# Kernel tuning notes

Measured on AMD Instinct MI355X. Metric: run time of the kernel, lower is better.

The kernel has to match this reference:

```python
import jax, jax.numpy as jnp
import numpy as np

B, N, D, E, H = 8, 256, 128, 32, 4
HD = D // H
EPS = 1e-5


def setup_inputs() -> dict:
    key = jax.random.key(0)
    ks = jax.random.split(key, 20)
    idx = jnp.arange(N)

    h = jax.random.normal(ks[0], (B, N, D), dtype=jnp.float32)
    adj = (jax.random.uniform(ks[1], (B, N, N)) < 0.5).astype(jnp.float32)
    adj = adj.at[:, idx, idx].set(1.0)
    edge_features = jax.random.normal(ks[2], (B, N, N, E), dtype=jnp.float32)
    src_mask = (jax.random.uniform(ks[3], (B, N, N)) < 0.7).astype(jnp.float32)
    src_mask = src_mask.at[:, idx, idx].set(1.0)

    s = 1.0 / np.sqrt(D)
    se = 1.0 / np.sqrt(E)
    p = {
        "gcn_w": jax.random.normal(ks[4], (D, D)) * s,
        "gcn_b": jnp.zeros((D,)),
        "edge_w": jax.random.normal(ks[5], (D, E)) * se,
        "edge_b": jnp.zeros((D,)),
        "wq": jax.random.normal(ks[6], (D, D)) * s,
        "wk": jax.random.normal(ks[7], (D, D)) * s,
        "wv": jax.random.normal(ks[8], (D, D)) * s,
        "bq": jnp.zeros((D,)),
        "bk": jnp.zeros((D,)),
        "bv": jnp.zeros((D,)),
        "out_w": jax.random.normal(ks[9], (D, D)) * s,
        "out_b": jnp.zeros((D,)),
        "ln_g": jnp.ones((D,)),
        "ln_b": jnp.zeros((D,)),
    }
    return {"h": h, "adj": adj, "edge_features": edge_features, "src_mask": src_mask, **p}


def reference(h, adj, edge_features, src_mask,
              gcn_w, gcn_b, edge_w, edge_b,
              wq, wk, wv, bq, bk, bv, out_w, out_b, ln_g, ln_b):
    b, n, d = h.shape

    # --- GCN branch: degree-normalized aggregation with self-loops ---
    adj_sl = adj + jnp.eye(n, dtype=h.dtype)[None]          # (B,N,N)
    deg = adj_sl.sum(-1, keepdims=True)                      # (B,N,1)
    h_agg = jnp.einsum('bnm,bmd->bnd', adj_sl, h) / deg
    h_gcn = h_agg @ gcn_w.T + gcn_b                          # (B,N,D)

    # --- edge-conditioned key/value: h_ij = h_j + edge_emb ---
    edge_emb = jnp.einsum('bnme,de->bnmd', edge_features, edge_w) + edge_b
    h_ij = h[:, None, :, :] + edge_emb                       # (B,N,N,D)

    # key padding mask: True where edge absent (masked)
    masked = (adj * src_mask) == 0                           # (B,N,N)

    # --- multi-head attention, one query per node ---
    q = (h @ wq.T + bq).reshape(b, n, H, HD)                 # (B,N,H,HD)
    k = (jnp.einsum('bnmd,ed->bnme', h_ij, wk) + bk).reshape(b, n, n, H, HD)
    v = (jnp.einsum('bnmd,ed->bnme', h_ij, wv) + bv).reshape(b, n, n, H, HD)

    scores = jnp.einsum('bnhd,bnmhd->bnhm', q, k) / np.sqrt(HD)  # (B,N,H,N)
    scores = jnp.where(masked[:, :, None, :], -jnp.inf, scores)
    attn = jax.nn.softmax(scores, axis=-1)
    o = jnp.einsum('bnhm,bnmhd->bnhd', attn, v).reshape(b, n, d)
    o = o @ out_w.T + out_b                                  # (B,N,D)

    # residual + layernorm (dropout is identity in eval)
    x = h + o
    mu = x.mean(-1, keepdims=True)
    var = ((x - mu) ** 2).mean(-1, keepdims=True)
    h_attn = ln_g * (x - mu) / jnp.sqrt(var + EPS) + ln_b

    return h_gcn + h_attn
```

## Files before the change

### kernel.cpp

```cpp
#include <hip/hip_runtime.h>
#include <hip/hip_bf16.h>

#define OFF_WQT 0
#define OFF_WKT 16384
#define OFF_WVT 32768
#define OFF_OWT 49152
#define OFF_GWT 65536
#define OFF_WKE 81920
#define OFF_WVE 86016
#define OFF_KB  90112
#define OFF_VB  90240
#define OFF_SC  90368
#define OFF_QS  98560
#define OFF_QE  360704
#define OFF_HA  622848
#define OFF_O   884992
#define OFF_K0  1147136
#define OFF_V0  1278208

static __device__ __forceinline__ float bflo(unsigned int w){
  union { unsigned int u; float f; } x; x.u = w << 16; return x.f;
}
static __device__ __forceinline__ float bfhi(unsigned int w){
  union { unsigned int u; float f; } x; x.u = w & 0xffff0000u; return x.f;
}
static __device__ __forceinline__ unsigned short f2bf(float f){
  union { float f; unsigned int u; } x; x.f = f;
  unsigned int r = (x.u + 0x7fffu + ((x.u >> 16) & 1u)) >> 16;
  return (unsigned short)r;
}

__global__ __launch_bounds__(256) void prep_kernel(
    const float* __restrict__ wq, const float* __restrict__ wk,
    const float* __restrict__ wv, const float* __restrict__ out_w,
    const float* __restrict__ gcn_w, const float* __restrict__ edge_w,
    const float* __restrict__ edge_b, const float* __restrict__ bk,
    const float* __restrict__ bv, float* __restrict__ ws)
{
  int blk = blockIdx.x, t = threadIdx.x;
  if (blk < 320) {
    int w = blk >> 6;
    int e0 = (blk & 63) * 256 + t;
    const float* src = (w==0) ? wq : (w==1) ? wk : (w==2) ? wv : (w==3) ? out_w : gcn_w;
    float* dst = ws + ((w==0) ? OFF_WQT : (w==1) ? OFF_WKT : (w==2) ? OFF_WVT
                      : (w==3) ? OFF_OWT : OFF_GWT);
    int k = e0 >> 7, d = e0 & 127;
    dst[e0] = src[d*128 + k];
  } else if (blk < 352) {
    int idx = blk - 320;
    int which = idx >> 4;
    int e0 = (idx & 15) * 256 + t;
    int d = e0 >> 5, e = e0 & 31;
    const float* W = which ? wv : wk;
    float acc = 0.f;
    #pragma unroll 4
    for (int k2 = 0; k2 < 128; ++k2) acc += W[d*128+k2] * edge_w[k2*32+e];
    ws[(which ? OFF_WVE : OFF_WKE) + e0] = acc;
  } else {
    int d = t & 127;
    const float* W  = (t < 128) ? wk : wv;
    const float* bb = (t < 128) ? bk : bv;
    float acc = bb[d];
    #pragma unroll 4
    for (int k2 = 0; k2 < 128; ++k2) acc += W[d*128+k2] * edge_b[k2];
    ws[((t < 128) ? OFF_KB : OFF_VB) + d] = acc;
  }
}

__global__ __launch_bounds__(256) void proj_kernel(
    const float* __restrict__ h, const float* __restrict__ bq,
    float* __restrict__ ws)
{
  __shared__ float part1[2][8][128];
  __shared__ float part2[2][8][128];
  __shared__ float part3[2][8][128];
  __shared__ float qrow[8*132];

  int t = threadIdx.x;
  int d = t & 127;
  int kh = __builtin_amdgcn_readfirstlane(t >> 7);
  int r0 = blockIdx.x * 8;

  const float* wqT = ws + OFF_WQT;
  const float* wkT = ws + OFF_WKT;
  const float* wvT = ws + OFF_WVT;

  float aq[8] = {0,0,0,0,0,0,0,0};
  float ak[8] = {0,0,0,0,0,0,0,0};
  float av[8] = {0,0,0,0,0,0,0,0};

  for (int kk = 0; kk < 64; ++kk) {
    int k = kh*64 + kk;
    float qw = wqT[k*128 + d];
    float kw = wkT[k*128 + d];
    float vw = wvT[k*128 + d];
    #pragma unroll
    for (int i = 0; i < 8; ++i) {
      float hv = h[(r0+i)*128 + k];
      aq[i] += qw * hv;
      ak[i] += kw * hv;
      av[i] += vw * hv;
    }
  }
  #pragma unroll
  for (int i = 0; i < 8; ++i) {
    part1[kh][i][d] = aq[i];
    part2[kh][i][d] = ak[i];
    part3[kh][i][d] = av[i];
  }
  __syncthreads();

  unsigned short* K0 = (unsigned short*)(ws + OFF_K0);
  unsigned short* V0 = (unsigned short*)(ws + OFF_V0);
  if (t < 128) {
    const float inv = 0.17677669529663687f;
    #pragma unroll
    for (int i = 0; i < 8; ++i) {
      float q  = (part1[0][i][d] + part1[1][i][d] + bq[d]) * inv;
      float k0 = part2[0][i][d] + part2[1][i][d];
      float v0 = part3[0][i][d] + part3[1][i][d];
      ws[OFF_QS + (r0+i)*128 + d] = q;
      qrow[i*132 + d] = q;
      K0[(r0+i)*128 + d] = f2bf(k0);
      V0[(r0+i)*128 + d] = f2bf(v0);
    }
  }
  __syncthreads();

  const float* Wke = ws + OFF_WKE;
  #pragma unroll
  for (int rep = 0; rep < 4; ++rep) {
    int flat = rep*256 + t;
    int i = flat >> 7, he = flat & 127;
    int hh = he >> 5, e = he & 31;
    float acc = 0.f;
    #pragma unroll
    for (int j = 0; j < 32; ++j)
      acc += Wke[(hh*32+j)*32 + e] * qrow[i*132 + hh*32 + j];
    ws[OFF_QE + (r0+i)*128 + he] = acc;
  }
  if (t < 32) {
    int i = t >> 2, hh = t & 3;
    float acc = 0.f;
    #pragma unroll
    for (int j = 0; j < 32; ++j)
      acc += qrow[i*132 + hh*32 + j] * ws[OFF_KB + hh*32 + j];
    ws[OFF_SC + (r0+i)*4 + hh] = acc;
  }
}

__global__ __launch_bounds__(256) void gcn_kernel(
    const float* __restrict__ h, const float* __restrict__ adj,
    float* __restrict__ ws)
{
  __shared__ float part[2][8][128];
  __shared__ float dpart[2][8];

  int t = threadIdx.x;
  int d = t & 127;
  int mh = __builtin_amdgcn_readfirstlane(t >> 7);
  int b = blockIdx.x >> 5;
  int n0 = (blockIdx.x & 31) * 8;

  float acc[8] = {0,0,0,0,0,0,0,0};
  float deg[8] = {0,0,0,0,0,0,0,0};
  for (int mm = 0; mm < 128; ++mm) {
    int m = mh*128 + mm;
    float hv = h[(b*256 + m)*128 + d];
    #pragma unroll
    for (int i = 0; i < 8; ++i) {
      float a = adj[(b*256 + n0 + i)*256 + m] + ((m == n0 + i) ? 1.0f : 0.0f);
      acc[i] += a * hv;
      deg[i] += a;
    }
  }
  #pragma unroll
  for (int i = 0; i < 8; ++i) part[mh][i][d] = acc[i];
  if (d == 0) {
    #pragma unroll
    for (int i = 0; i < 8; ++i) dpart[mh][i] = deg[i];
  }
  __syncthreads();
  if (t < 128) {
    #pragma unroll
    for (int i = 0; i < 8; ++i) {
      float s  = part[0][i][d] + part[1][i][d];
      float dg = dpart[0][i] + dpart[1][i];
      ws[OFF_HA + (b*256 + n0 + i)*128 + d] = s / dg;
    }
  }
}

__global__ __launch_bounds__(256) void attn_kernel(
    const float* __restrict__ edge, const float* __restrict__ adj,
    const float* __restrict__ srcm, const float* __restrict__ ws,
    float* __restrict__ obuf)
{
  __shared__ float e_lds[256*36];
  __shared__ float s_lds[4*264];
  __shared__ float red[8];
  __shared__ float part[16*132];
  __shared__ float ebar[128];

  int t  = threadIdx.x;
  int bn = blockIdx.x;
  int b  = bn >> 8;

  const float* qs = ws + OFF_QS + (size_t)bn*128;
  const float* qe = ws + OFF_QE + (size_t)bn*128;
  const float* sc = ws + OFF_SC + (size_t)bn*4;
  const unsigned short* K0 = (const unsigned short*)(ws + OFF_K0);
  const unsigned short* V0 = (const unsigned short*)(ws + OFF_V0);

  int m = t;
  float4 ev[8];
  {
    const float4* ep = (const float4*)(edge + ((size_t)bn*256 + (size_t)m)*32);
    #pragma unroll
    for (int j = 0; j < 8; ++j) ev[j] = ep[j];
    float* erow = e_lds + m*36;
    #pragma unroll
    for (int j = 0; j < 8; ++j) ((float4*)erow)[j] = ev[j];
  }

  float s4[4];
  {
    const uint4* kv = (const uint4*)(K0 + (size_t)(b*256 + m)*128);
    #pragma unroll
    for (int hh = 0; hh < 4; ++hh) {
      float acc = sc[hh];
      #pragma unroll
      for (int q4 = 0; q4 < 4; ++q4) {
        uint4 kw = kv[hh*4 + q4];
        const float* qp = qs + hh*32 + q4*8;
        acc += qp[0]*bflo(kw.x) + qp[1]*bfhi(kw.x)
             + qp[2]*bflo(kw.y) + qp[3]*bfhi(kw.y)
             + qp[4]*bflo(kw.z) + qp[5]*bfhi(kw.z)
             + qp[6]*bflo(kw.w) + qp[7]*bfhi(kw.w);
      }
      const float* qep = qe + hh*32;
      #pragma unroll
      for (int j = 0; j < 8; ++j) {
        acc += qep[4*j+0]*ev[j].x + qep[4*j+1]*ev[j].y
             + qep[4*j+2]*ev[j].z + qep[4*j+3]*ev[j].w;
      }
      s4[hh] = acc;
    }
    float ma = adj[(size_t)bn*256 + m];
    float ms = srcm[(size_t)bn*256 + m];
    if (ma * ms == 0.0f) { s4[0] = s4[1] = s4[2] = s4[3] = -1e30f; }
    #pragma unroll
    for (int hh = 0; hh < 4; ++hh) s_lds[hh*264 + m] = s4[hh];
  }
  __syncthreads();

  {
    int wvh = t >> 6, ln = t & 63;
    float v0 = s_lds[wvh*264 + ln];
    float v1 = s_lds[wvh*264 + ln + 64];
    float v2 = s_lds[wvh*264 + ln + 128];
    float v3 = s_lds[wvh*264 + ln + 192];
    float mx = fmaxf(fmaxf(v0, v1), fmaxf(v2, v3));
    #pragma unroll
    for (int off = 32; off > 0; off >>= 1) mx = fmaxf(mx, __shfl_down(mx, off));
    mx = __shfl(mx, 0);
    float sm = __expf(v0-mx) + __expf(v1-mx) + __expf(v2-mx) + __expf(v3-mx);
    #pragma unroll
    for (int off = 32; off > 0; off >>= 1) sm += __shfl_down(sm, off);
    if (ln == 0) { red[wvh] = mx; red[4+wvh] = 1.0f / sm; }
  }
  __syncthreads();

  {
    #pragma unroll
    for (int hh = 0; hh < 4; ++hh) {
      float a = __expf(s4[hh] - red[hh]) * red[4+hh];
      s_lds[hh*264 + m] = a;
    }
  }
  __syncthreads();

  {
    int ms = t >> 5, hh = (t >> 3) & 3, e4 = t & 7;
    float4 acc = {0,0,0,0};
    for (int jm = 0; jm < 32; ++jm) {
      int mm = ms*32 + jm;
      float a = s_lds[hh*264 + mm];
      float4 evv = *(const float4*)(e_lds + mm*36 + e4*4);
      acc.x += a*evv.x; acc.y += a*evv.y; acc.z += a*evv.z; acc.w += a*evv.w;
    }
    *(float4*)(part + ms*132 + hh*32 + e4*4) = acc;
  }
  __syncthreads();
  if (t < 128) {
    float s2 = 0.f;
    #pragma unroll
    for (int ms = 0; ms < 8; ++ms) s2 += part[ms*132 + t];
    ebar[t] = s2;
  }
  __syncthreads();

  {
    int ms = t >> 4, hh = (t >> 2) & 3, dg = t & 3;
    float a0=0,a1=0,a2=0,a3=0,a4=0,a5=0,a6=0,a7=0;
    const uint4* vb = (const uint4*)(V0 + (size_t)b*256*128);
    int colq = hh*4 + dg;
    for (int jm = 0; jm < 16; ++jm) {
      int mm = ms*16 + jm;
      float a = s_lds[hh*264 + mm];
      uint4 vw = vb[mm*16 + colq];
      a0 += a*bflo(vw.x); a1 += a*bfhi(vw.x);
      a2 += a*bflo(vw.y); a3 += a*bfhi(vw.y);
      a4 += a*bflo(vw.z); a5 += a*bfhi(vw.z);
      a6 += a*bflo(vw.w); a7 += a*bfhi(vw.w);
    }
    float* pp = part + ms*132 + hh*32 + dg*8;
    pp[0]=a0; pp[1]=a1; pp[2]=a2; pp[3]=a3; pp[4]=a4; pp[5]=a5; pp[6]=a6; pp[7]=a7;
  }
  __syncthreads();

  if (t < 128) {
    float s2 = 0.f;
    #pragma unroll
    for (int ms = 0; ms < 16; ++ms) s2 += part[ms*132 + t];
    int hh = t >> 5;
    float acc = s2 + ws[OFF_VB + t];
    const float* wve = ws + OFF_WVE + t*32;
    #pragma unroll
    for (int e = 0; e < 32; ++e) acc += wve[e] * ebar[hh*32 + e];
    obuf[(size_t)bn*128 + t] = acc;
  }
}

__global__ __launch_bounds__(256) void final_kernel(
    const float* __restrict__ h, const float* __restrict__ ws,
    const float* __restrict__ out_b, const float* __restrict__ ln_g,
    const float* __restrict__ ln_b, const float* __restrict__ gcn_b,
    float* __restrict__ out)
{
  __shared__ float p1[2][8][128];
  __shared__ float p2[2][8][128];
  __shared__ float xl[8*132];
  __shared__ float stat[16];

  int t = threadIdx.x;
  int d = t & 127;
  int kh = __builtin_amdgcn_readfirstlane(t >> 7);
  int r0 = blockIdx.x * 8;

  const float* owT = ws + OFF_OWT;
  const float* gwT = ws + OFF_GWT;
  const float* ob  = ws + OFF_O;
  const float* ha  = ws + OFF_HA;

  float xa[8] = {0,0,0,0,0,0,0,0};
  float ga[8] = {0,0,0,0,0,0,0,0};
  for (int kk = 0; kk < 64; ++kk) {
    int k = kh*64 + kk;
    float ow = owT[k*128 + d];
    float gw = gwT[k*128 + d];
    #pragma unroll
    for (int i = 0; i < 8; ++i) {
      xa[i] += ow * ob[(r0+i)*128 + k];
      ga[i] += gw * ha[(r0+i)*128 + k];
    }
  }
  #pragma unroll
  for (int i = 0; i < 8; ++i) { p1[kh][i][d] = xa[i]; p2[kh][i][d] = ga[i]; }
  __syncthreads();

  float gtot[8];
  if (t < 128) {
    #pragma unroll
    for (int i = 0; i < 8; ++i) {
      float x = p1[0][i][d] + p1[1][i][d] + out_b[d] + h[(r0+i)*128 + d];
      xl[i*132 + d] = x;
      gtot[i] = p2[0][i][d] + p2[1][i][d];
    }
  }
  __syncthreads();

  {
    int i = t >> 5, l = t & 31;
    float s = 0.f, ss = 0.f;
    #pragma unroll
    for (int j = 0; j < 4; ++j) {
      float x = xl[i*132 + l + 32*j];
      s += x; ss += x*x;
    }
    #pragma unroll
    for (int off = 16; off > 0; off >>= 1) {
      s  += __shfl_down(s,  off, 32);
      ss += __shfl_down(ss, off, 32);
    }
    if (l == 0) {
      float mu  = s * (1.0f/128.0f);
      float var = ss * (1.0f/128.0f) - mu*mu;
      stat[i]   = mu;
      stat[8+i] = rsqrtf(var + 1e-5f);
    }
  }
  __syncthreads();

  if (t < 128) {
    #pragma unroll
    for (int i = 0; i < 8; ++i) {
      float mu = stat[i], rs = stat[8+i];
      float x  = xl[i*132 + d];
      out[(r0+i)*128 + d] = ln_g[d]*(x-mu)*rs + ln_b[d] + gtot[i] + gcn_b[d];
    }
  }
}

extern "C" void kernel_launch(void* const* d_in, const int* in_sizes, int n_in,
                              void* d_out, int out_size, void* d_ws, size_t ws_size,
                              hipStream_t stream) {
  (void)in_sizes; (void)n_in; (void)out_size; (void)ws_size;
  const float* h     = (const float*)d_in[0];
  const float* adj   = (const float*)d_in[1];
  const float* edge  = (const float*)d_in[2];
  const float* srcm  = (const float*)d_in[3];
  const float* gcn_w = (const float*)d_in[4];
  const float* gcn_b = (const float*)d_in[5];
  const float* edge_w= (const float*)d_in[6];
  const float* edge_b= (const float*)d_in[7];
  const float* wq    = (const float*)d_in[8];
  const float* wk    = (const float*)d_in[9];
  const float* wv    = (const float*)d_in[10];
  const float* bq    = (const float*)d_in[11];
  const float* bk    = (const float*)d_in[12];
  const float* bv    = (const float*)d_in[13];
  const float* out_w = (const float*)d_in[14];
  const float* out_b = (const float*)d_in[15];
  const float* ln_g  = (const float*)d_in[16];
  const float* ln_b  = (const float*)d_in[17];

  float* ws  = (float*)d_ws;
  float* out = (float*)d_out;

  prep_kernel<<<353, 256, 0, stream>>>(wq, wk, wv, out_w, gcn_w, edge_w, edge_b, bk, bv, ws);
  proj_kernel<<<256, 256, 0, stream>>>(h, bq, ws);
  gcn_kernel<<<256, 256, 0, stream>>>(h, adj, ws);
  attn_kernel<<<2048, 256, 0, stream>>>(edge, adj, srcm, ws, ws + OFF_O);
  final_kernel<<<256, 256, 0, stream>>>(h, ws, out_b, ln_g, ln_b, gcn_b, out);
}
```

Measured before the change: 229.2 us.

## Fuse GCN into final kernel, merge attention reductions, bf16 edge tile in LDS

Removes the separate GCN kernel and computes the degree-normalized aggregation inside the final kernel, so the h_agg workspace round-trip and one launch go away. The attention kernel stores edge features in LDS as bf16 and runs the edge-weighted and V reductions in one loop with fewer barriers, with a launch-bounds occupancy hint. Projection and final kernels switch to 4 rows per block with twice as many blocks, and h and adj rows are staged in LDS. The bf16 edge features add rounding error to the attention output, and the final kernel now carries the full GCN aggregation work.

```diff
diff --git a/kernel.cpp b/kernel.cpp
--- a/kernel.cpp
+++ b/kernel.cpp
@@ -13,7 +13,6 @@
 #define OFF_SC  90368
 #define OFF_QS  98560
 #define OFF_QE  360704
-#define OFF_HA  622848
 #define OFF_O   884992
 #define OFF_K0  1147136
 #define OFF_V0  1278208
@@ -71,23 +70,27 @@
     const float* __restrict__ h, const float* __restrict__ bq,
     float* __restrict__ ws)
 {
-  __shared__ float part1[2][8][128];
-  __shared__ float part2[2][8][128];
-  __shared__ float part3[2][8][128];
-  __shared__ float qrow[8*132];
+  __shared__ float h_lds[512];
+  __shared__ float p1[2][4][128];
+  __shared__ float p2[2][4][128];
+  __shared__ float p3[2][4][128];
+  __shared__ float qrow[4*132];
 
   int t = threadIdx.x;
   int d = t & 127;
-  int kh = __builtin_amdgcn_readfirstlane(t >> 7);
-  int r0 = blockIdx.x * 8;
+  int kh = t >> 7;
+  int r0 = blockIdx.x * 4;
+
+  if (t < 128) ((float4*)h_lds)[t] = ((const float4*)(h + (size_t)r0*128))[t];
+  __syncthreads();
 
   const float* wqT = ws + OFF_WQT;
   const float* wkT = ws + OFF_WKT;
   const float* wvT = ws + OFF_WVT;
 
-  float aq[8] = {0,0,0,0,0,0,0,0};
-  float ak[8] = {0,0,0,0,0,0,0,0};
-  float av[8] = {0,0,0,0,0,0,0,0};
+  float aq[4] = {0,0,0,0};
+  float ak[4] = {0,0,0,0};
+  float av[4] = {0,0,0,0};
 
   for (int kk = 0; kk < 64; ++kk) {
     int k = kh*64 + kk;
@@ -95,18 +98,18 @@
     float kw = wkT[k*128 + d];
     float vw = wvT[k*128 + d];
     #pragma unroll
-    for (int i = 0; i < 8; ++i) {
-      float hv = h[(r0+i)*128 + k];
+    for (int i = 0; i < 4; ++i) {
+      float hv = h_lds[i*128 + k];
       aq[i] += qw * hv;
       ak[i] += kw * hv;
       av[i] += vw * hv;
     }
   }
   #pragma unroll
-  for (int i = 0; i < 8; ++i) {
-    part1[kh][i][d] = aq[i];
-    part2[kh][i][d] = ak[i];
-    part3[kh][i][d] = av[i];
+  for (int i = 0; i < 4; ++i) {
+    p1[kh][i][d] = aq[i];
+    p2[kh][i][d] = ak[i];
+    p3[kh][i][d] = av[i];
   }
   __syncthreads();
 
@@ -115,21 +118,21 @@
   if (t < 128) {
     const float inv = 0.17677669529663687f;
     #pragma unroll
-    for (int i = 0; i < 8; ++i) {
-      float q  = (part1[0][i][d] + part1[1][i][d] + bq[d]) * inv;
-      float k0 = part2[0][i][d] + part2[1][i][d];
-      float v0 = part3[0][i][d] + part3[1][i][d];
-      ws[OFF_QS + (r0+i)*128 + d] = q;
+    for (int i = 0; i < 4; ++i) {
+      float q  = (p1[0][i][d] + p1[1][i][d] + bq[d]) * inv;
+      float k0 = p2[0][i][d] + p2[1][i][d];
+      float v0 = p3[0][i][d] + p3[1][i][d];
+      ws[OFF_QS + (size_t)(r0+i)*128 + d] = q;
       qrow[i*132 + d] = q;
-      K0[(r0+i)*128 + d] = f2bf(k0);
-      V0[(r0+i)*128 + d] = f2bf(v0);
+      K0[(size_t)(r0+i)*128 + d] = f2bf(k0);
+      V0[(size_t)(r0+i)*128 + d] = f2bf(v0);
     }
   }
   __syncthreads();
 
   const float* Wke = ws + OFF_WKE;
   #pragma unroll
-  for (int rep = 0; rep < 4; ++rep) {
+  for (int rep = 0; rep < 2; ++rep) {
     int flat = rep*256 + t;
     int i = flat >> 7, he = flat & 127;
     int hh = he >> 5, e = he & 31;
@@ -137,70 +140,29 @@
     #pragma unroll
     for (int j = 0; j < 32; ++j)
       acc += Wke[(hh*32+j)*32 + e] * qrow[i*132 + hh*32 + j];
-    ws[OFF_QE + (r0+i)*128 + he] = acc;
-  }
-  if (t < 32) {
+    ws[OFF_QE + (size_t)(r0+i)*128 + he] = acc;
+  }
+  if (t < 16) {
     int i = t >> 2, hh = t & 3;
     float acc = 0.f;
     #pragma unroll
     for (int j = 0; j < 32; ++j)
       acc += qrow[i*132 + hh*32 + j] * ws[OFF_KB + hh*32 + j];
-    ws[OFF_SC + (r0+i)*4 + hh] = acc;
-  }
-}
-
-__global__ __launch_bounds__(256) void gcn_kernel(
-    const float* __restrict__ h, const float* __restrict__ adj,
-    float* __restrict__ ws)
-{
-  __shared__ float part[2][8][128];
-  __shared__ float dpart[2][8];
-
-  int t = threadIdx.x;
-  int d = t & 127;
-  int mh = __builtin_amdgcn_readfirstlane(t >> 7);
-  int b = blockIdx.x >> 5;
-  int n0 = (blockIdx.x & 31) * 8;
-
-  float acc[8] = {0,0,0,0,0,0,0,0};
-  float deg[8] = {0,0,0,0,0,0,0,0};
-  for (int mm = 0; mm < 128; ++mm) {
-    int m = mh*128 + mm;
-    float hv = h[(b*256 + m)*128 + d];
-    #pragma unroll
-    for (int i = 0; i < 8; ++i) {
-      float a = adj[(b*256 + n0 + i)*256 + m] + ((m == n0 + i) ? 1.0f : 0.0f);
-      acc[i] += a * hv;
-      deg[i] += a;
-    }
-  }
-  #pragma unroll
-  for (int i = 0; i < 8; ++i) part[mh][i][d] = acc[i];
-  if (d == 0) {
-    #pragma unroll
-    for (int i = 0; i < 8; ++i) dpart[mh][i] = deg[i];
-  }
-  __syncthreads();
-  if (t < 128) {
-    #pragma unroll
-    for (int i = 0; i < 8; ++i) {
-      float s  = part[0][i][d] + part[1][i][d];
-      float dg = dpart[0][i] + dpart[1][i];
-      ws[OFF_HA + (b*256 + n0 + i)*128 + d] = s / dg;
-    }
-  }
-}
-
-__global__ __launch_bounds__(256) void attn_kernel(
+    ws[OFF_SC + (size_t)(r0+i)*4 + hh] = acc;
+  }
+}
+
+__global__ __launch_bounds__(256, 4) void attn_kernel(
     const float* __restrict__ edge, const float* __restrict__ adj,
     const float* __restrict__ srcm, const float* __restrict__ ws,
     float* __restrict__ obuf)
 {
-  __shared__ float e_lds[256*36];
-  __shared__ float s_lds[4*264];
+  __shared__ unsigned int e_bf[256*18];
+  __shared__ float s_lds[1028];
+  __shared__ float part4[8*132];
+  __shared__ float part5[8*132];
+  __shared__ float ebar[128];
   __shared__ float red[8];
-  __shared__ float part[16*132];
-  __shared__ float ebar[128];
 
   int t  = threadIdx.x;
   int bn = blockIdx.x;
@@ -210,17 +172,24 @@
   const float* qe = ws + OFF_QE + (size_t)bn*128;
   const float* sc = ws + OFF_SC + (size_t)bn*4;
   const unsigned short* K0 = (const unsigned short*)(ws + OFF_K0);
-  const unsigned short* V0 = (const unsigned short*)(ws + OFF_V0);
+  const unsigned int*  V0u = (const unsigned int*)(ws + OFF_V0);
 
   int m = t;
+  float ma = adj[(size_t)bn*256 + m];
+  float msk = srcm[(size_t)bn*256 + m];
   float4 ev[8];
   {
     const float4* ep = (const float4*)(edge + ((size_t)bn*256 + (size_t)m)*32);
     #pragma unroll
     for (int j = 0; j < 8; ++j) ev[j] = ep[j];
-    float* erow = e_lds + m*36;
-    #pragma unroll
-    for (int j = 0; j < 8; ++j) ((float4*)erow)[j] = ev[j];
+    unsigned int* erow = e_bf + m*18;
+    #pragma unroll
+    for (int j = 0; j < 8; ++j) {
+      uint2 pk;
+      pk.x = (unsigned int)f2bf(ev[j].x) | ((unsigned int)f2bf(ev[j].y) << 16);
+      pk.y = (unsigned int)f2bf(ev[j].z) | ((unsigned int)f2bf(ev[j].w) << 16);
+      *(uint2*)(erow + j*2) = pk;
+    }
   }
 
   float s4[4];
@@ -246,20 +215,18 @@
       }
       s4[hh] = acc;
     }
-    float ma = adj[(size_t)bn*256 + m];
-    float ms = srcm[(size_t)bn*256 + m];
-    if (ma * ms == 0.0f) { s4[0] = s4[1] = s4[2] = s4[3] = -1e30f; }
-    #pragma unroll
-    for (int hh = 0; hh < 4; ++hh) s_lds[hh*264 + m] = s4[hh];
+    if (ma * msk == 0.0f) { s4[0] = s4[1] = s4[2] = s4[3] = -1e30f; }
+    #pragma unroll
+    for (int hh = 0; hh < 4; ++hh) s_lds[hh*257 + m] = s4[hh];
   }
   __syncthreads();
 
   {
     int wvh = t >> 6, ln = t & 63;
-    float v0 = s_lds[wvh*264 + ln];
-    float v1 = s_lds[wvh*264 + ln + 64];
-    float v2 = s_lds[wvh*264 + ln + 128];
-    float v3 = s_lds[wvh*264 + ln + 192];
+    float v0 = s_lds[wvh*257 + ln];
+    float v1 = s_lds[wvh*257 + ln + 64];
+    float v2 = s_lds[wvh*257 + ln + 128];
+    float v3 = s_lds[wvh*257 + ln + 192];
     float mx = fmaxf(fmaxf(v0, v1), fmaxf(v2, v3));
     #pragma unroll
     for (int off = 32; off > 0; off >>= 1) mx = fmaxf(mx, __shfl_down(mx, off));
@@ -271,58 +238,46 @@
   }
   __syncthreads();
 
-  {
-    #pragma unroll
-    for (int hh = 0; hh < 4; ++hh) {
-      float a = __expf(s4[hh] - red[hh]) * red[4+hh];
-      s_lds[hh*264 + m] = a;
-    }
-  }
-  __syncthreads();
-
-  {
-    int ms = t >> 5, hh = (t >> 3) & 3, e4 = t & 7;
-    float4 acc = {0,0,0,0};
+  #pragma unroll
+  for (int hh = 0; hh < 4; ++hh)
+    s_lds[hh*257 + m] = __expf(s4[hh] - red[hh]) * red[4+hh];
+  __syncthreads();
+
+  {
+    int ms  = t >> 5;
+    int hh4 = (t >> 3) & 3, e4 = t & 7;
+    int c   = t & 31,  hh5 = c >> 3;
+    float p4x=0,p4y=0,p4z=0,p4w=0;
+    float p5x=0,p5y=0,p5z=0,p5w=0;
+    const unsigned int* vrow = V0u + (size_t)b*256*64;
     for (int jm = 0; jm < 32; ++jm) {
       int mm = ms*32 + jm;
-      float a = s_lds[hh*264 + mm];
-      float4 evv = *(const float4*)(e_lds + mm*36 + e4*4);
-      acc.x += a*evv.x; acc.y += a*evv.y; acc.z += a*evv.z; acc.w += a*evv.w;
-    }
-    *(float4*)(part + ms*132 + hh*32 + e4*4) = acc;
-  }
-  __syncthreads();
-  if (t < 128) {
-    float s2 = 0.f;
-    #pragma unroll
-    for (int ms = 0; ms < 8; ++ms) s2 += part[ms*132 + t];
-    ebar[t] = s2;
-  }
-  __syncthreads();
-
-  {
-    int ms = t >> 4, hh = (t >> 2) & 3, dg = t & 3;
-    float a0=0,a1=0,a2=0,a3=0,a4=0,a5=0,a6=0,a7=0;
-    const uint4* vb = (const uint4*)(V0 + (size_t)b*256*128);
-    int colq = hh*4 + dg;
-    for (int jm = 0; jm < 16; ++jm) {
-      int mm = ms*16 + jm;
-      float a = s_lds[hh*264 + mm];
-      uint4 vw = vb[mm*16 + colq];
-      a0 += a*bflo(vw.x); a1 += a*bfhi(vw.x);
-      a2 += a*bflo(vw.y); a3 += a*bfhi(vw.y);
-      a4 += a*bflo(vw.z); a5 += a*bfhi(vw.z);
-      a6 += a*bflo(vw.w); a7 += a*bfhi(vw.w);
-    }
-    float* pp = part + ms*132 + hh*32 + dg*8;
-    pp[0]=a0; pp[1]=a1; pp[2]=a2; pp[3]=a3; pp[4]=a4; pp[5]=a5; pp[6]=a6; pp[7]=a7;
-  }
-  __syncthreads();
-
-  if (t < 128) {
-    float s2 = 0.f;
-    #pragma unroll
-    for (int ms = 0; ms < 16; ++ms) s2 += part[ms*132 + t];
+      float a4 = s_lds[hh4*257 + mm];
+      uint2 w = *(const uint2*)(e_bf + mm*18 + e4*2);
+      p4x += a4*bflo(w.x); p4y += a4*bfhi(w.x);
+      p4z += a4*bflo(w.y); p4w += a4*bfhi(w.y);
+      float a5 = s_lds[hh5*257 + mm];
+      uint2 vv = *(const uint2*)(vrow + (size_t)mm*64 + c*2);
+      p5x += a5*bflo(vv.x); p5y += a5*bfhi(vv.x);
+      p5z += a5*bflo(vv.y); p5w += a5*bfhi(vv.y);
+    }
+    float4 f4; f4.x=p4x; f4.y=p4y; f4.z=p4z; f4.w=p4w;
+    *(float4*)(part4 + ms*132 + hh4*32 + e4*4) = f4;
+    float4 f5; f5.x=p5x; f5.y=p5y; f5.z=p5z; f5.w=p5w;
+    *(float4*)(part5 + ms*132 + c*4) = f5;
+  }
+  __syncthreads();
+
+  float s2 = 0.f;
+  if (t < 128) {
+    float se = 0.f;
+    #pragma unroll
+    for (int g = 0; g < 8; ++g) { se += part4[g*132 + t]; s2 += part5[g*132 + t]; }
+    ebar[t] = se;
+  }
+  __syncthreads();
+
+  if (t < 128) {
     int hh = t >> 5;
     float acc = s2 + ws[OFF_VB + t];
     const float* wve = ws + OFF_WVE + t*32;
@@ -333,81 +288,115 @@
 }
 
 __global__ __launch_bounds__(256) void final_kernel(
-    const float* __restrict__ h, const float* __restrict__ ws,
-    const float* __restrict__ out_b, const float* __restrict__ ln_g,
-    const float* __restrict__ ln_b, const float* __restrict__ gcn_b,
-    float* __restrict__ out)
+    const float* __restrict__ h, const float* __restrict__ adj,
+    const float* __restrict__ ws, const float* __restrict__ out_b,
+    const float* __restrict__ ln_g, const float* __restrict__ ln_b,
+    const float* __restrict__ gcn_b, float* __restrict__ out)
 {
-  __shared__ float p1[2][8][128];
-  __shared__ float p2[2][8][128];
-  __shared__ float xl[8*132];
-  __shared__ float stat[16];
+  __shared__ float adj_lds[1024];
+  __shared__ float o_lds[512];
+  __shared__ float ha_lds[4*132];
+  __shared__ float pa[2][4][128];
+  __shared__ float pb[2][4][128];
+  __shared__ float dpart[2][4];
+  __shared__ float xl[4*132];
+  __shared__ float stat[8];
 
   int t = threadIdx.x;
   int d = t & 127;
-  int kh = __builtin_amdgcn_readfirstlane(t >> 7);
-  int r0 = blockIdx.x * 8;
-
-  const float* owT = ws + OFF_OWT;
-  const float* gwT = ws + OFF_GWT;
-  const float* ob  = ws + OFF_O;
-  const float* ha  = ws + OFF_HA;
-
-  float xa[8] = {0,0,0,0,0,0,0,0};
-  float ga[8] = {0,0,0,0,0,0,0,0};
-  for (int kk = 0; kk < 64; ++kk) {
-    int k = kh*64 + kk;
-    float ow = owT[k*128 + d];
-    float gw = gwT[k*128 + d];
-    #pragma unroll
-    for (int i = 0; i < 8; ++i) {
-      xa[i] += ow * ob[(r0+i)*128 + k];
-      ga[i] += gw * ha[(r0+i)*128 + k];
-    }
-  }
-  #pragma unroll
-  for (int i = 0; i < 8; ++i) { p1[kh][i][d] = xa[i]; p2[kh][i][d] = ga[i]; }
-  __syncthreads();
-
-  float gtot[8];
-  if (t < 128) {
-    #pragma unroll
-    for (int i = 0; i < 8; ++i) {
-      float x = p1[0][i][d] + p1[1][i][d] + out_b[d] + h[(r0+i)*128 + d];
+  int kh = t >> 7;
+  int b  = blockIdx.x >> 6;
+  int n0 = (blockIdx.x & 63) * 4;
+  int r0 = b*256 + n0;
+
+  ((float4*)adj_lds)[t] = ((const float4*)(adj + (size_t)r0*256))[t];
+  if (t < 128) ((float4*)o_lds)[t] = ((const float4*)(ws + OFF_O + (size_t)r0*128))[t];
+  __syncthreads();
+
+  {
+    float ag[4] = {0,0,0,0};
+    float dg[4] = {0,0,0,0};
+    for (int mm = 0; mm < 128; ++mm) {
+      int mloc = kh*128 + mm;
+      float hv = h[((size_t)b*256 + mloc)*128 + d];
+      #pragma unroll
+      for (int i = 0; i < 4; ++i) {
+        float a = adj_lds[i*256 + mloc] + ((mloc == n0 + i) ? 1.0f : 0.0f);
+        ag[i] += a * hv;
+        dg[i] += a;
+      }
+    }
+    #pragma unroll
+    for (int i = 0; i < 4; ++i) pa[kh][i][d] = ag[i];
+    if (d == 0) {
+      #pragma unroll
+      for (int i = 0; i < 4; ++i) dpart[kh][i] = dg[i];
+    }
+  }
+  __syncthreads();
+  if (t < 128) {
+    #pragma unroll
+    for (int i = 0; i < 4; ++i)
+      ha_lds[i*132 + d] = (pa[0][i][d] + pa[1][i][d]) / (dpart[0][i] + dpart[1][i]);
+  }
+  __syncthreads();
+
+  {
+    const float* owT = ws + OFF_OWT;
+    const float* gwT = ws + OFF_GWT;
+    float xa[4] = {0,0,0,0};
+    float ga[4] = {0,0,0,0};
+    for (int kk = 0; kk < 64; ++kk) {
+      int k = kh*64 + kk;
+      float ow = owT[k*128 + d];
+      float gw = gwT[k*128 + d];
+      #pragma unroll
+      for (int i = 0; i < 4; ++i) {
+        xa[i] += ow * o_lds[i*128 + k];
+        ga[i] += gw * ha_lds[i*132 + k];
+      }
+    }
+    #pragma unroll
+    for (int i = 0; i < 4; ++i) { pa[kh][i][d] = xa[i]; pb[kh][i][d] = ga[i]; }
+  }
+  __syncthreads();
+
+  float gtot[4];
+  if (t < 128) {
+    #pragma unroll
+    for (int i = 0; i < 4; ++i) {
+      float x = pa[0][i][d] + pa[1][i][d] + out_b[d] + h[(size_t)(r0+i)*128 + d];
       xl[i*132 + d] = x;
-      gtot[i] = p2[0][i][d] + p2[1][i][d];
-    }
-  }
-  __syncthreads();
-
-  {
-    int i = t >> 5, l = t & 31;
-    float s = 0.f, ss = 0.f;
-    #pragma unroll
-    for (int j = 0; j < 4; ++j) {
-      float x = xl[i*132 + l + 32*j];
-      s += x; ss += x*x;
-    }
-    #pragma unroll
-    for (int off = 16; off > 0; off >>= 1) {
-      s  += __shfl_down(s,  off, 32);
-      ss += __shfl_down(ss, off, 32);
+      gtot[i] = pb[0][i][d] + pb[1][i][d];
+    }
+  }
+  __syncthreads();
+
+  {
+    int i = t >> 6, l = t & 63;
+    float x0 = xl[i*132 + l];
+    float x1 = xl[i*132 + l + 64];
+    float s = x0 + x1, ss = x0*x0 + x1*x1;
+    #pragma unroll
+    for (int off = 32; off > 0; off >>= 1) {
+      s  += __shfl_down(s,  off);
+      ss += __shfl_down(ss, off);
     }
     if (l == 0) {
       float mu  = s * (1.0f/128.0f);
       float var = ss * (1.0f/128.0f) - mu*mu;
       stat[i]   = mu;
-      stat[8+i] = rsqrtf(var + 1e-5f);
-    }
-  }
-  __syncthreads();
-
-  if (t < 128) {
-    #pragma unroll
-    for (int i = 0; i < 8; ++i) {
-      float mu = stat[i], rs = stat[8+i];
-      float x  = xl[i*132 + d];
-      out[(r0+i)*128 + d] = ln_g[d]*(x-mu)*rs + ln_b[d] + gtot[i] + gcn_b[d];
+      stat[4+i] = rsqrtf(var + 1e-5f);
+    }
+  }
+  __syncthreads();
+
+  if (t < 128) {
+    #pragma unroll
+    for (int i = 0; i < 4; ++i) {
+      float x = xl[i*132 + d];
+      out[(size_t)(r0+i)*128 + d] =
+          ln_g[d]*(x - stat[i])*stat[4+i] + ln_b[d] + gtot[i] + gcn_b[d];
     }
   }
 }
@@ -439,8 +428,7 @@
   float* out = (float*)d_out;
 
   prep_kernel<<<353, 256, 0, stream>>>(wq, wk, wv, out_w, gcn_w, edge_w, edge_b, bk, bv, ws);
-  proj_kernel<<<256, 256, 0, stream>>>(h, bq, ws);
-  gcn_kernel<<<256, 256, 0, stream>>>(h, adj, ws);
+  proj_kernel<<<512, 256, 0, stream>>>(h, bq, ws);
   attn_kernel<<<2048, 256, 0, stream>>>(edge, adj, srcm, ws, ws + OFF_O);
-  final_kernel<<<256, 256, 0, stream>>>(h, ws, out_b, ln_g, ln_b, gcn_b, out);
-}
+  final_kernel<<<512, 256, 0, stream>>>(h, adj, ws, out_b, ln_g, ln_b, gcn_b, out);
+}
```

After: 197.5 us. -13.8%, faster.
